# Performance work log

Measured on AMD Instinct MI355X. Metric: run time of the kernel, lower is better.

The kernel has to match this reference:

```python
import jax, jax.numpy as jnp
import numpy as np

N_NODES = 50000
N_EDGES = 500000
IN_CH = 2
HID = 64
OUT_CH = 64
H1 = 4
H2 = 1
EDGE_DIM = 2


def _glorot(key, shape):
    fan_in, fan_out = shape[0], shape[1]
    lim = jnp.sqrt(6.0 / (fan_in + fan_out))
    return jax.random.uniform(key, shape, jnp.float32, -lim, lim)


def setup_inputs() -> dict:
    key = jax.random.key(0)
    ks = jax.random.split(key, 16)
    x = jax.random.uniform(ks[0], (N_NODES, IN_CH), jnp.float32)
    edge_index = jax.random.randint(ks[1], (2, N_EDGES), 0, N_NODES, dtype=jnp.int64)
    edge_attr = jax.random.uniform(ks[2], (N_EDGES, EDGE_DIM), jnp.float32)
    batch = jnp.zeros((N_NODES,), jnp.int32)
    # conv1 params (GATv2: lin_l, lin_r with bias, lin_edge no bias, att, out bias)
    W1l = _glorot(ks[3], (IN_CH, H1 * HID)); b1l = jnp.zeros((H1 * HID,), jnp.float32)
    W1r = _glorot(ks[4], (IN_CH, H1 * HID)); b1r = jnp.zeros((H1 * HID,), jnp.float32)
    W1e = _glorot(ks[5], (EDGE_DIM, H1 * HID))
    att1 = _glorot(ks[6], (H1, HID))
    bias1 = jnp.zeros((H1 * HID,), jnp.float32)
    # conv2 params
    W2l = _glorot(ks[7], (H1 * HID, H2 * OUT_CH)); b2l = jnp.zeros((H2 * OUT_CH,), jnp.float32)
    W2r = _glorot(ks[8], (H1 * HID, H2 * OUT_CH)); b2r = jnp.zeros((H2 * OUT_CH,), jnp.float32)
    W2e = _glorot(ks[9], (EDGE_DIM, H2 * OUT_CH))
    att2 = _glorot(ks[10], (H2, OUT_CH))
    bias2 = jnp.zeros((H2 * OUT_CH,), jnp.float32)
    return dict(x=x, edge_attr=edge_attr,
                W1l=W1l, b1l=b1l, W1r=W1r, b1r=b1r, W1e=W1e, att1=att1, bias1=bias1,
                W2l=W2l, b2l=b2l, W2r=W2r, b2r=b2r, W2e=W2e, att2=att2, bias2=bias2,
                edge_index=edge_index, batch=batch)


def _segment_softmax(alpha, seg, num_segments):
    # alpha: [E, H], seg: [E] destination ids
    amax = jax.ops.segment_max(alpha, seg, num_segments=num_segments)
    amax = jnp.where(jnp.isfinite(amax), amax, 0.0)
    ex = jnp.exp(alpha - amax[seg])
    denom = jax.ops.segment_sum(ex, seg, num_segments=num_segments)
    return ex / (denom[seg] + 1e-16)


def _gatv2_conv(x, edge_index, edge_attr, Wl, bl, Wr, br, We, att, bias, heads, out_c):
    N = x.shape[0]
    src, dst = edge_index[0], edge_index[1]
    # add self loops with fill_value='mean' for edge_attr (PyG default)
    ones = jnp.ones((src.shape[0],), x.dtype)
    deg = jax.ops.segment_sum(ones, dst, num_segments=N)
    loop_attr = jax.ops.segment_sum(edge_attr, dst, num_segments=N) / jnp.maximum(deg, 1.0)[:, None]
    loops = jnp.arange(N, dtype=src.dtype)
    src = jnp.concatenate([src, loops])
    dst = jnp.concatenate([dst, loops])
    ea = jnp.concatenate([edge_attr, loop_attr], axis=0)
    xl = (x @ Wl + bl).reshape(N, heads, out_c)   # source-side transform
    xr = (x @ Wr + br).reshape(N, heads, out_c)   # target-side transform
    ee = (ea @ We).reshape(-1, heads, out_c)
    e = jax.nn.leaky_relu(xl[src] + xr[dst] + ee, 0.2)   # [E', H, C]
    alpha = jnp.einsum('ehc,hc->eh', e, att)
    alpha = _segment_softmax(alpha, dst, N)
    out = jax.ops.segment_sum(xl[src] * alpha[..., None], dst, num_segments=N)
    return out.reshape(N, heads * out_c) + bias


def reference(x, edge_attr, W1l, b1l, W1r, b1r, W1e, att1, bias1,
              W2l, b2l, W2r, b2r, W2e, att2, bias2, edge_index, batch):
    h = jax.nn.elu(_gatv2_conv(x, edge_index, edge_attr, W1l, b1l, W1r, b1r, W1e, att1, bias1, H1, HID))
    # dropout skipped (eval mode)
    h = _gatv2_conv(h, edge_index, edge_attr, W2l, b2l, W2r, b2r, W2e, att2, bias2, H2, OUT_CH)
    # global_mean_pool over batch (single graph -> [1, OUT_CH])
    nb = 1
    cnt = jax.ops.segment_sum(jnp.ones((h.shape[0],), h.dtype), batch, num_segments=nb)
    pooled = jax.ops.segment_sum(h, batch, num_segments=nb) / jnp.maximum(cnt, 1.0)[:, None]
    return pooled
```

## Files before the change

kernel.cpp:

```cpp
#include <hip/hip_runtime.h>
#include <hip/hip_bf16.h>

#define N_NODES 50000
#define N_EDGES 500000
#define E_AUG   (N_EDGES + N_NODES)
#define NH1 4
#define HID 64
#define C2  64

#define NBUCK  196
#define BNODES 256
#define BCAP   4096

#define NL2B    2048
#define L2CHUNK 272
#define L2BINS  320

typedef unsigned int uint32;
typedef unsigned short ushort16;
typedef __attribute__((ext_vector_type(8))) short short8v;
typedef __attribute__((ext_vector_type(4))) float f32x4;

__device__ __forceinline__ ushort16 f2bf(float f) {
    union { float f; uint32 u; } v; v.f = f;
    uint32 u = v.u + (0x7FFFu + ((v.u >> 16) & 1u));
    return (ushort16)(u >> 16);
}
__device__ __forceinline__ float bf2f(ushort16 h) {
    union { uint32 u; float f; } v; v.u = ((uint32)h) << 16;
    return v.f;
}


__global__ void zero_bcnt_kernel(int* __restrict__ bcnt) {
    if (threadIdx.x < 256) bcnt[threadIdx.x] = 0;
}


#define PACK_BLOCKS 128
#define HIST_BLOCKS ((N_EDGES / 4 + 255) / 256)

__global__ void pass1_kernel(const int* __restrict__ ei, const float* __restrict__ ea,
                             const float* __restrict__ W1l, const float* __restrict__ b1l,
                             const float* __restrict__ W1r, const float* __restrict__ b1r,
                             const float* __restrict__ W1e, const float* __restrict__ att1,
                             const float* __restrict__ bias1,
                             const float* __restrict__ W2l, const float* __restrict__ W2r,
                             float* __restrict__ Wpack, float* __restrict__ Apack,
                             float4* __restrict__ wpk4, ushort16* __restrict__ Wt,
                             int4* __restrict__ stage, int* __restrict__ bcnt) {
    const int tid = threadIdx.x;
    if (blockIdx.x < PACK_BLOCKS) {
        int t = blockIdx.x * 256 + tid;
        if (blockIdx.x == 0) {
            if (tid < 256) {
                int h = tid >> 6, hc = tid;
                float* wp = &Wpack[((tid & 63) * 4 + h) * 8];
                wp[0] = W1l[hc];       wp[1] = W1l[256 + hc];
                wp[2] = W1r[hc];       wp[3] = W1r[256 + hc];
                wp[4] = W1e[hc];       wp[5] = W1e[256 + hc];
                wp[6] = b1l[hc] + b1r[hc];
                wp[7] = 0.4f * att1[hc];
                wpk4[hc] = make_float4(W1l[hc], W1l[256 + hc], b1l[hc] + bias1[hc], 0.0f);
            }
            if (tid < 28) {
                int h = tid / 7, comp = tid % 7;
                float s = 0.0f;
                for (int c = 0; c < 64; ++c) {
                    int hc = h * 64 + c;
                    float m;
                    switch (comp) {
                        case 0: m = W1l[hc]; break;
                        case 1: m = W1l[256 + hc]; break;
                        case 2: m = W1r[hc]; break;
                        case 3: m = W1r[256 + hc]; break;
                        case 4: m = W1e[hc]; break;
                        case 5: m = W1e[256 + hc]; break;
                        default: m = b1l[hc] + b1r[hc]; break;
                    }
                    s += att1[hc] * m;
                }
                Apack[h * 8 + comp] = 0.6f * s;
            }
        }
        if (t < 128 * 256) {
            int c = t & 127, k = t >> 7;
            float w = (c < 64) ? W2l[k * 64 + c] : W2r[k * 64 + (c - 64)];
            Wt[c * 256 + k] = f2bf(w);
        }
    } else {
        __shared__ int lbc[NBUCK];
        __shared__ int lbase[NBUCK];
        if (tid < NBUCK) lbc[tid] = 0;
        __syncthreads();

        const int e0 = ((blockIdx.x - PACK_BLOCKS) * 256 + tid) * 4;
        int4 rec[4]; int bket[4], lofs[4];
        bool val[4];
        #pragma unroll
        for (int j = 0; j < 4; ++j) {
            const int e = e0 + j;
            val[j] = (e < N_EDGES);
            if (val[j]) {
                int s = ei[e], d = ei[N_EDGES + e];
                float2 a = *(const float2*)&ea[2 * e];
                rec[j].x = s; rec[j].y = d;
                rec[j].z = __float_as_int(a.x); rec[j].w = __float_as_int(a.y);
                bket[j] = d >> 8;
                lofs[j] = atomicAdd(&lbc[bket[j]], 1);
            }
        }
        __syncthreads();
        if (tid < NBUCK) lbase[tid] = lbc[tid] ? atomicAdd(&bcnt[tid], lbc[tid]) : 0;
        __syncthreads();
        #pragma unroll
        for (int j = 0; j < 4; ++j)
            if (val[j])
                stage[bket[j] * BCAP + lbase[bket[j]] + lofs[j]] = rec[j];
    }
}


__global__ void bscan_kernel(const int* __restrict__ bcnt, int* __restrict__ bbase,
                             int* __restrict__ offs) {
    __shared__ int s[256];
    int tid = threadIdx.x;
    int nodec = (tid < NBUCK) ? min(BNODES, N_NODES - tid * BNODES) : 0;
    int v = (tid < NBUCK) ? bcnt[tid] + nodec : 0;
    s[tid] = v;
    __syncthreads();
    for (int off = 1; off < 256; off <<= 1) {
        int t = (tid >= off) ? s[tid - off] : 0;
        __syncthreads();
        s[tid] += t;
        __syncthreads();
    }
    if (tid < NBUCK) bbase[tid] = s[tid] - v;
    if (tid == 0) offs[N_NODES] = E_AUG;
}


__global__ __launch_bounds__(256) void buildk_kernel(
    const int4* __restrict__ stage, const int* __restrict__ bcnt,
    const int* __restrict__ bbase,
    int* __restrict__ offs, float* __restrict__ den,
    int4* __restrict__ epk, int* __restrict__ e_src) {
    __shared__ int bins[256];
    __shared__ float ls0[256], ls1[256];
    __shared__ int scan[256];
    __shared__ int cursor[256];
    const int tid = threadIdx.x, bk = blockIdx.x;
    bins[tid] = 0; ls0[tid] = 0.0f; ls1[tid] = 0.0f;
    __syncthreads();

    const int n_ = bcnt[bk];
    const int4* sb = stage + (size_t)bk * BCAP;
    for (int i = tid; i < n_; i += 256) {
        int4 r = sb[i];
        int li = r.y & 255;
        atomicAdd(&bins[li], 1);
        atomicAdd(&ls0[li], __int_as_float(r.z));
        atomicAdd(&ls1[li], __int_as_float(r.w));
    }
    __syncthreads();

    const int node = bk * BNODES + tid;
    const int v = (node < N_NODES) ? bins[tid] + 1 : 0;
    scan[tid] = v;
    __syncthreads();
    for (int off = 1; off < 256; off <<= 1) {
        int t = (tid >= off) ? scan[tid - off] : 0;
        __syncthreads();
        scan[tid] += t;
        __syncthreads();
    }
    const int o = bbase[bk] + scan[tid] - v;
    if (node < N_NODES) {
        offs[node] = o;
        den[node] = 0.0f;
        float dgf = (float)max(bins[tid], 1);
        int4 sl;
        sl.x = node; sl.y = node;
        sl.z = __float_as_int(ls0[tid] / dgf);
        sl.w = __float_as_int(ls1[tid] / dgf);
        epk[o] = sl;
        e_src[o] = node;
    }
    cursor[tid] = o + 1;
    __syncthreads();

    for (int i = tid; i < n_; i += 256) {
        int4 r = sb[i];
        int pos = atomicAdd(&cursor[r.y & 255], 1);
        epk[pos] = r;
        e_src[pos] = r.x;
    }
}


__global__ __launch_bounds__(256) void l1_alpha_kernel(
    const float* __restrict__ x, const int4* __restrict__ epk,
    const float* __restrict__ Wpack, const float* __restrict__ Apack,
    float* __restrict__ alpha1) {
    __shared__ float sWp[2048];
    __shared__ float sA[32];
    const int tid = threadIdx.x;
    for (int i = tid; i < 2048; i += 256) sWp[i] = Wpack[i];
    if (tid < 32) sA[tid] = Apack[tid];
    __syncthreads();

    const int e0 = (blockIdx.x * 256 + tid) * 2;
    if (e0 >= E_AUG) return;

    const int4 v0 = epk[e0];
    const int4 v1 = epk[e0 + 1];

    float u0[2], u1[2], u2[2], u3[2], u4[2], u5[2];
    {
        const float2 xs0 = *(const float2*)&x[2 * v0.x];
        const float2 xd0 = *(const float2*)&x[2 * v0.y];
        const float2 xs1 = *(const float2*)&x[2 * v1.x];
        const float2 xd1 = *(const float2*)&x[2 * v1.y];
        u0[0] = xs0.x; u1[0] = xs0.y; u2[0] = xd0.x; u3[0] = xd0.y;
        u4[0] = __int_as_float(v0.z); u5[0] = __int_as_float(v0.w);
        u0[1] = xs1.x; u1[1] = xs1.y; u2[1] = xd1.x; u3[1] = xd1.y;
        u4[1] = __int_as_float(v1.z); u5[1] = __int_as_float(v1.w);
    }

    float p[4][2];
    #pragma unroll
    for (int h = 0; h < 4; ++h) {
        const float a0 = sA[h * 8], a1 = sA[h * 8 + 1], a2 = sA[h * 8 + 2],
                    a3 = sA[h * 8 + 3], a4 = sA[h * 8 + 4], a5 = sA[h * 8 + 5],
                    a6 = sA[h * 8 + 6];
        #pragma unroll
        for (int j = 0; j < 2; ++j)
            p[h][j] = fmaf(u0[j], a0, fmaf(u1[j], a1, fmaf(u2[j], a2,
                      fmaf(u3[j], a3, fmaf(u4[j], a4, fmaf(u5[j], a5, a6))))));
    }

    for (int c = 0; c < 64; ++c) {
        const float* wp = &sWp[c * 32];
        #pragma unroll
        for (int h = 0; h < 4; ++h) {
            const float4 wa = *(const float4*)&wp[h * 8];
            const float4 wb = *(const float4*)&wp[h * 8 + 4];
            #pragma unroll
            for (int j = 0; j < 2; ++j) {
                float t = fmaf(u0[j], wa.x,
                          fmaf(u1[j], wa.y,
                          fmaf(u2[j], wa.z,
                          fmaf(u3[j], wa.w,
                          fmaf(u4[j], wb.x,
                          fmaf(u5[j], wb.y, wb.z))))));
                p[h][j] = fmaf(fabsf(t), wb.w, p[h][j]);
            }
        }
    }

    #pragma unroll
    for (int h = 0; h < 4; ++h)
        *(float2*)&alpha1[(size_t)h * E_AUG + e0] =
            make_float2(__expf(p[h][0]), __expf(p[h][1]));
}


__global__ __launch_bounds__(256) void l1out_fused_kernel(
    const float* __restrict__ x, const int* __restrict__ offs,
    const int* __restrict__ e_src, const float* __restrict__ alpha1,
    const float4* __restrict__ wpk4, const ushort16* __restrict__ Wt,
    const float* __restrict__ b2l, const float* __restrict__ b2r,
    ushort16* __restrict__ xl2b, ushort16* __restrict__ xr2b) {
    __shared__ short hlds[64 * 256];
    __shared__ float4 swpk[256];
    const int tid = threadIdx.x;
    const int n0 = blockIdx.x * 64;
    const int lane = tid & 63, w = tid >> 6;

    swpk[tid] = wpk4[tid];

    const int nl = tid >> 2, head = tid & 3;
    const int node = n0 + nl;
    float S1 = 0.0f, S2 = 0.0f;
    if (node < N_NODES) {
        const int beg = offs[node], end = offs[node + 1];
        const float* ap = alpha1 + (size_t)head * E_AUG;
        float den = 0.0f, s1 = 0.0f, s2 = 0.0f;
        for (int e = beg; e < end; ++e) {
            float wt = ap[e];
            int s = e_src[e];
            float2 xs = *(const float2*)&x[2 * s];
            den += wt;
            s1 = fmaf(wt, xs.x, s1);
            s2 = fmaf(wt, xs.y, s2);
        }
        float inv = 1.0f / (den + 1e-16f);
        S1 = s1 * inv;
        S2 = s2 * inv;
    }
    __syncthreads();

    {
        const int kseg = head * 64;
        const int swz = (nl & 7) << 3;
        for (int i = 0; i < 8; ++i) {
            short8v hv;
            #pragma unroll
            for (int j = 0; j < 8; ++j) {
                float4 wv = swpk[kseg + i * 8 + j];
                float g = fmaf(wv.x, S1, fmaf(wv.y, S2, wv.z));
                g = g > 0.0f ? g : (__expf(g) - 1.0f);
                hv[j] = (short)f2bf(g);
            }
            *(short8v*)&hlds[(nl * 256 + kseg + i * 8) ^ swz] = hv;
        }
    }

    short8v bfrag[2][8];
    {
        const int bc = w * 32 + (lane & 15);
        const int k0 = (lane >> 4) * 8;
        #pragma unroll
        for (int ct = 0; ct < 2; ++ct)
            #pragma unroll
            for (int kb = 0; kb < 8; ++kb)
                bfrag[ct][kb] = *(const short8v*)&Wt[(size_t)(bc + ct * 16) * 256 + kb * 32 + k0];
    }
    __syncthreads();

    f32x4 acc[4][2];
    #pragma unroll
    for (int rt = 0; rt < 4; ++rt)
        #pragma unroll
        for (int ct = 0; ct < 2; ++ct)
            acc[rt][ct] = (f32x4){0.0f, 0.0f, 0.0f, 0.0f};

    const int arow = lane & 15, ak0 = (lane >> 4) * 8;
    #pragma unroll
    for (int rt = 0; rt < 4; ++rt) {
        const int n = rt * 16 + arow;
        const int swz = (n & 7) << 3;
        #pragma unroll
        for (int kb = 0; kb < 8; ++kb) {
            short8v a = *(const short8v*)&hlds[(n * 256 + kb * 32 + ak0) ^ swz];
            acc[rt][0] = __builtin_amdgcn_mfma_f32_16x16x32_bf16(a, bfrag[0][kb], acc[rt][0], 0, 0, 0);
            acc[rt][1] = __builtin_amdgcn_mfma_f32_16x16x32_bf16(a, bfrag[1][kb], acc[rt][1], 0, 0, 0);
        }
    }

    #pragma unroll
    for (int ct = 0; ct < 2; ++ct) {
        const int c = w * 32 + ct * 16 + (lane & 15);
        const bool isL = (c < 64);
        const int cc = isL ? c : c - 64;
        const float bias = isL ? b2l[cc] : b2r[cc];
        ushort16* dst = isL ? xl2b : xr2b;
        #pragma unroll
        for (int rt = 0; rt < 4; ++rt)
            #pragma unroll
            for (int r = 0; r < 4; ++r) {
                int nn = n0 + rt * 16 + (lane >> 4) * 4 + r;
                if (nn < N_NODES) dst[nn * 64 + cc] = f2bf(acc[rt][ct][r] + bias);
            }
    }
}


__global__ __launch_bounds__(256) void l2_logit_kernel(
    const ushort16* __restrict__ xl2b, const ushort16* __restrict__ xr2b,
    const int4* __restrict__ epk,
    const float* __restrict__ W2e, const float* __restrict__ att2,
    float* __restrict__ alpha2, float* __restrict__ den) {
    __shared__ float sWe[128], satt[64];
    __shared__ float bins[L2BINS];
    const int tid = threadIdx.x;
    if (tid < 128) sWe[tid] = W2e[tid];
    if (tid < 64) satt[tid] = att2[tid];
    for (int i = tid; i < L2BINS; i += 256) bins[i] = 0.0f;
    const int base = blockIdx.x * L2CHUNK;
    const int d_first = epk[min(base, E_AUG - 1)].y;
    __syncthreads();

    const int lane = tid & 63, w = tid >> 6;
    const int cl = lane & 15, g = lane >> 4;
    const uint32* xlp = (const uint32*)xl2b;
    const uint32* xrp = (const uint32*)xr2b;

    for (int it = 0; it < L2CHUNK / 16; ++it) {
        const int e = base + it * 16 + w * 4 + g;
        if (e < E_AUG) {
            const int4 v = epk[e];
            const float ae0 = __int_as_float(v.z), ae1 = __int_as_float(v.w);
            float acc = 0.0f;
            #pragma unroll
            for (int q = 0; q < 2; ++q) {
                const int c2 = cl + q * 16;
                const uint32 ul = xlp[v.x * 32 + c2];
                const uint32 ur = xrp[v.y * 32 + c2];
                const int c0 = 2 * c2, c1 = 2 * c2 + 1;
                float xl0 = bf2f((ushort16)(ul & 0xffff)), xl1 = bf2f((ushort16)(ul >> 16));
                float xr0 = bf2f((ushort16)(ur & 0xffff)), xr1 = bf2f((ushort16)(ur >> 16));
                float t0 = xl0 + xr0 + fmaf(ae0, sWe[c0], ae1 * sWe[64 + c0]);
                float t1 = xl1 + xr1 + fmaf(ae0, sWe[c1], ae1 * sWe[64 + c1]);
                t0 = t0 > 0.0f ? t0 : 0.2f * t0;
                t1 = t1 > 0.0f ? t1 : 0.2f * t1;
                acc = fmaf(t0, satt[c0], fmaf(t1, satt[c1], acc));
            }
            #pragma unroll
            for (int off = 8; off; off >>= 1) acc += __shfl_xor(acc, off);
            if (cl == 0) {
                float wv = __expf(acc);
                alpha2[e] = wv;
                int rel = v.y - d_first;
                if (rel < L2BINS) atomicAdd(&bins[rel], wv);
                else atomicAdd(&den[v.y], wv);
            }
        }
    }
    __syncthreads();
    for (int i = tid; i < L2BINS; i += 256) {
        float b = bins[i];
        int node = d_first + i;
        if (b != 0.0f && node < N_NODES) atomicAdd(&den[node], b);
    }
}


__global__ __launch_bounds__(256) void l2_pool_kernel(
    const ushort16* __restrict__ xl2b, const int4* __restrict__ epk,
    const float* __restrict__ alpha2, const float* __restrict__ den,
    float* __restrict__ pblock) {
    __shared__ float sp[16][64];
    const int tid = threadIdx.x;
    const int lane = tid & 63, w = tid >> 6;
    const int cl = lane & 15, g = lane >> 4;
    const int slot = w * 4 + g;
    const int base = blockIdx.x * L2CHUNK;
    const uint32* xlp = (const uint32*)xl2b;

    float a0 = 0.0f, a1 = 0.0f, a2 = 0.0f, a3 = 0.0f;
    for (int it = 0; it < L2CHUNK / 16; ++it) {
        const int e = base + it * 16 + w * 4 + g;
        if (e < E_AUG) {
            const int4 v = epk[e];
            const float coef = alpha2[e] / (den[v.y] + 1e-16f);
            const uint32 u0 = xlp[v.x * 32 + cl];
            const uint32 u1 = xlp[v.x * 32 + cl + 16];
            a0 = fmaf(coef, bf2f((ushort16)(u0 & 0xffff)), a0);
            a1 = fmaf(coef, bf2f((ushort16)(u0 >> 16)), a1);
            a2 = fmaf(coef, bf2f((ushort16)(u1 & 0xffff)), a2);
            a3 = fmaf(coef, bf2f((ushort16)(u1 >> 16)), a3);
        }
    }
    sp[slot][2 * cl] = a0;
    sp[slot][2 * cl + 1] = a1;
    sp[slot][2 * cl + 32] = a2;
    sp[slot][2 * cl + 33] = a3;
    __syncthreads();
    if (tid < 64) {
        float s = 0.0f;
        #pragma unroll
        for (int i = 0; i < 16; ++i) s += sp[i][tid];
        pblock[blockIdx.x * 64 + tid] = s;
    }
}


__global__ __launch_bounds__(256) void pool_partial_kernel(const float* __restrict__ pblock,
                                                           float* __restrict__ pfin) {
    __shared__ float s[256];
    int tid = threadIdx.x;
    int l = tid & 63, q = tid >> 6;
    float local = 0.0f;
    for (int r = blockIdx.x * 4 + q; r < NL2B; r += 64 * 4)
        local += pblock[r * 64 + l];
    s[tid] = local;
    __syncthreads();
    if (tid < 64) {
        float v = s[tid] + s[tid + 64] + s[tid + 128] + s[tid + 192];
        pfin[blockIdx.x * 64 + tid] = v;
    }
}

__global__ __launch_bounds__(256) void pool_final2_kernel(const float* __restrict__ pfin,
                                                          const float* __restrict__ bias2,
                                                          float* __restrict__ d_out) {
    __shared__ float s[256];
    int tid = threadIdx.x;
    int l = tid & 63, q = tid >> 6;
    float local = 0.0f;
    for (int r = q; r < 64; r += 4)
        local += pfin[r * 64 + l];
    s[tid] = local;
    __syncthreads();
    if (tid < 64) {
        float v = s[tid] + s[tid + 64] + s[tid + 128] + s[tid + 192];
        d_out[tid] = v * (1.0f / N_NODES) + bias2[tid];
    }
}


extern "C" void kernel_launch(void* const* d_in, const int* in_sizes, int n_in,
                              void* d_out, int out_size, void* d_ws, size_t ws_size,
                              hipStream_t stream) {
    const float* x     = (const float*)d_in[0];
    const float* eattr = (const float*)d_in[1];
    const float* W1l   = (const float*)d_in[2];
    const float* b1l   = (const float*)d_in[3];
    const float* W1r   = (const float*)d_in[4];
    const float* b1r   = (const float*)d_in[5];
    const float* W1e   = (const float*)d_in[6];
    const float* att1  = (const float*)d_in[7];
    const float* bias1 = (const float*)d_in[8];
    const float* W2l   = (const float*)d_in[9];
    const float* b2l   = (const float*)d_in[10];
    const float* W2r   = (const float*)d_in[11];
    const float* b2r   = (const float*)d_in[12];
    const float* W2e   = (const float*)d_in[13];
    const float* att2  = (const float*)d_in[14];
    const float* bias2 = (const float*)d_in[15];
    const int*   ei    = (const int*)d_in[16];
    float* out = (float*)d_out;

    char* p = (char*)d_ws;
    auto alloc = [&](size_t bytes) -> void* {
        void* r = (void*)p;
        p += (bytes + 255) & ~(size_t)255;
        return r;
    };
    int*   bcnt   = (int*)alloc(256 * 4);
    int*   bbase  = (int*)alloc(256 * 4);
    int*   offs   = (int*)alloc((N_NODES + 1) * 4);
    float* den    = (float*)alloc(N_NODES * 4);
    int4*  stage  = (int4*)alloc((size_t)NBUCK * BCAP * 16);
    int4*  epk    = (int4*)alloc((size_t)E_AUG * 16);
    int*   e_src  = (int*)alloc(E_AUG * 4);
    float* alpha1 = (float*)alloc((size_t)E_AUG * 4 * 4);
    float* alpha2 = (float*)alloc((size_t)E_AUG * 4);
    float* Wpack  = (float*)alloc(256 * 8 * 4);
    float* Apack  = (float*)alloc(32 * 4);
    float4* wpk4  = (float4*)alloc(256 * 16);
    ushort16* Wt  = (ushort16*)alloc(128 * 256 * 2);
    ushort16* xl2b = (ushort16*)alloc((size_t)N_NODES * C2 * 2);
    ushort16* xr2b = (ushort16*)alloc((size_t)N_NODES * C2 * 2);
    float* pblock = (float*)alloc((size_t)NL2B * 64 * 4);
    float* pfin   = (float*)alloc((size_t)64 * 64 * 4);

    zero_bcnt_kernel<<<1, 256, 0, stream>>>(bcnt);

    pass1_kernel<<<PACK_BLOCKS + HIST_BLOCKS, 256, 0, stream>>>(
        ei, eattr, W1l, b1l, W1r, b1r, W1e, att1, bias1, W2l, W2r,
        Wpack, Apack, wpk4, Wt, stage, bcnt);

    bscan_kernel<<<1, 256, 0, stream>>>(bcnt, bbase, offs);

    buildk_kernel<<<NBUCK, 256, 0, stream>>>(stage, bcnt, bbase, offs, den, epk, e_src);

    l1_alpha_kernel<<<(E_AUG / 2 + 255) / 256, 256, 0, stream>>>(x, epk, Wpack, Apack,
                                                                 alpha1);

    l1out_fused_kernel<<<(N_NODES + 63) / 64, 256, 0, stream>>>(x, offs, e_src, alpha1,
                                                                wpk4, Wt, b2l, b2r,
                                                                xl2b, xr2b);

    l2_logit_kernel<<<NL2B, 256, 0, stream>>>(xl2b, xr2b, epk, W2e, att2, alpha2, den);

    l2_pool_kernel<<<NL2B, 256, 0, stream>>>(xl2b, epk, alpha2, den, pblock);

    pool_partial_kernel<<<64, 256, 0, stream>>>(pblock, pfin);
    pool_final2_kernel<<<1, 256, 0, stream>>>(pfin, bias2, out);
}
```

Before: 179.8 us.

## Fuse layer-1 attention logits into edge bucketing pass and self-loops into aggregation

Computes the layer-1 per-edge exp-logits for all four heads inside the bucketing pass and carries them through the CSR build as a packed float4 array. Self-loop logits are now computed directly in the node aggregation kernel, so the separate l1_alpha kernel goes away. Weight packing and the zeroing of the bucket counter are split into their own prep kernel, which runs ahead of the bucketing pass. This saves a kernel launch and a re-read of epk with scattered x gathers. The cost is an extra 16-byte staging write and read per edge, plus more shared memory and a longer per-thread workload in the pass1 and l1out kernels.

New measurement: 206.6 us. 1.15x slower.

```diff
diff --git a/kernel.cpp b/kernel.cpp
--- a/kernel.cpp
+++ b/kernel.cpp
@@ -32,92 +32,123 @@
 }
 
 
-__global__ void zero_bcnt_kernel(int* __restrict__ bcnt) {
-    if (threadIdx.x < 256) bcnt[threadIdx.x] = 0;
-}
-
-
-#define PACK_BLOCKS 128
+__global__ void prep_kernel(const float* __restrict__ W1l, const float* __restrict__ b1l,
+                            const float* __restrict__ W1r, const float* __restrict__ b1r,
+                            const float* __restrict__ W1e, const float* __restrict__ att1,
+                            const float* __restrict__ bias1,
+                            const float* __restrict__ W2l, const float* __restrict__ W2r,
+                            float* __restrict__ Wpack, float* __restrict__ Apack,
+                            float4* __restrict__ wpk4, ushort16* __restrict__ Wt,
+                            int* __restrict__ bcnt) {
+    const int tid = threadIdx.x;
+    int t = blockIdx.x * 256 + tid;
+    if (blockIdx.x == 0) {
+        bcnt[tid] = 0;
+        {
+            int h = tid >> 6, hc = tid;
+            float* wp = &Wpack[((tid & 63) * 4 + h) * 8];
+            wp[0] = W1l[hc];       wp[1] = W1l[256 + hc];
+            wp[2] = W1r[hc];       wp[3] = W1r[256 + hc];
+            wp[4] = W1e[hc];       wp[5] = W1e[256 + hc];
+            wp[6] = b1l[hc] + b1r[hc];
+            wp[7] = 0.4f * att1[hc];
+            wpk4[hc] = make_float4(W1l[hc], W1l[256 + hc], b1l[hc] + bias1[hc], 0.0f);
+        }
+        if (tid < 28) {
+            int h = tid / 7, comp = tid % 7;
+            float s = 0.0f;
+            for (int c = 0; c < 64; ++c) {
+                int hc = h * 64 + c;
+                float m;
+                switch (comp) {
+                    case 0: m = W1l[hc]; break;
+                    case 1: m = W1l[256 + hc]; break;
+                    case 2: m = W1r[hc]; break;
+                    case 3: m = W1r[256 + hc]; break;
+                    case 4: m = W1e[hc]; break;
+                    case 5: m = W1e[256 + hc]; break;
+                    default: m = b1l[hc] + b1r[hc]; break;
+                }
+                s += att1[hc] * m;
+            }
+            Apack[h * 8 + comp] = 0.6f * s;
+        }
+    }
+    if (t < 128 * 256) {
+        int c = t & 127, k = t >> 7;
+        float w = (c < 64) ? W2l[k * 64 + c] : W2r[k * 64 + (c - 64)];
+        Wt[c * 256 + k] = f2bf(w);
+    }
+}
+
+
 #define HIST_BLOCKS ((N_EDGES / 4 + 255) / 256)
 
-__global__ void pass1_kernel(const int* __restrict__ ei, const float* __restrict__ ea,
-                             const float* __restrict__ W1l, const float* __restrict__ b1l,
-                             const float* __restrict__ W1r, const float* __restrict__ b1r,
-                             const float* __restrict__ W1e, const float* __restrict__ att1,
-                             const float* __restrict__ bias1,
-                             const float* __restrict__ W2l, const float* __restrict__ W2r,
-                             float* __restrict__ Wpack, float* __restrict__ Apack,
-                             float4* __restrict__ wpk4, ushort16* __restrict__ Wt,
-                             int4* __restrict__ stage, int* __restrict__ bcnt) {
+__global__ __launch_bounds__(256) void pass1_kernel(
+    const int* __restrict__ ei, const float* __restrict__ ea,
+    const float* __restrict__ x,
+    const float* __restrict__ Wpack, const float* __restrict__ Apack,
+    int4* __restrict__ st_meta, float4* __restrict__ st_alpha,
+    int* __restrict__ bcnt) {
+    __shared__ float sWp[2048];
+    __shared__ float sA[32];
+    __shared__ int lbc[NBUCK];
+    __shared__ int lbase[NBUCK];
     const int tid = threadIdx.x;
-    if (blockIdx.x < PACK_BLOCKS) {
-        int t = blockIdx.x * 256 + tid;
-        if (blockIdx.x == 0) {
-            if (tid < 256) {
-                int h = tid >> 6, hc = tid;
-                float* wp = &Wpack[((tid & 63) * 4 + h) * 8];
-                wp[0] = W1l[hc];       wp[1] = W1l[256 + hc];
-                wp[2] = W1r[hc];       wp[3] = W1r[256 + hc];
-                wp[4] = W1e[hc];       wp[5] = W1e[256 + hc];
-                wp[6] = b1l[hc] + b1r[hc];
-                wp[7] = 0.4f * att1[hc];
-                wpk4[hc] = make_float4(W1l[hc], W1l[256 + hc], b1l[hc] + bias1[hc], 0.0f);
+    for (int i = tid; i < 2048; i += 256) sWp[i] = Wpack[i];
+    if (tid < 32) sA[tid] = Apack[tid];
+    if (tid < NBUCK) lbc[tid] = 0;
+    __syncthreads();
+
+    const int e0 = (blockIdx.x * 256 + tid) * 4;
+    int4 rec[4]; float4 al[4]; int bket[4], lofs[4];
+    bool val[4];
+    #pragma unroll
+    for (int j = 0; j < 4; ++j) {
+        const int e = e0 + j;
+        val[j] = (e < N_EDGES);
+        if (val[j]) {
+            const int s = ei[e], d = ei[N_EDGES + e];
+            const float2 a = *(const float2*)&ea[2 * e];
+            rec[j].x = s; rec[j].y = d;
+            rec[j].z = __float_as_int(a.x); rec[j].w = __float_as_int(a.y);
+            bket[j] = d >> 8;
+            lofs[j] = atomicAdd(&lbc[bket[j]], 1);
+
+            const float2 xs = *(const float2*)&x[2 * s];
+            const float2 xd = *(const float2*)&x[2 * d];
+            const float u0 = xs.x, u1 = xs.y, u2 = xd.x, u3 = xd.y, u4 = a.x, u5 = a.y;
+
+            float p[4];
+            #pragma unroll
+            for (int h = 0; h < 4; ++h)
+                p[h] = fmaf(u0, sA[h * 8], fmaf(u1, sA[h * 8 + 1], fmaf(u2, sA[h * 8 + 2],
+                       fmaf(u3, sA[h * 8 + 3], fmaf(u4, sA[h * 8 + 4],
+                       fmaf(u5, sA[h * 8 + 5], sA[h * 8 + 6]))))));
+            for (int c = 0; c < 64; ++c) {
+                const float* wp = &sWp[c * 32];
+                #pragma unroll
+                for (int h = 0; h < 4; ++h) {
+                    const float4 wa = *(const float4*)&wp[h * 8];
+                    const float4 wb = *(const float4*)&wp[h * 8 + 4];
+                    float tt = fmaf(u0, wa.x, fmaf(u1, wa.y, fmaf(u2, wa.z,
+                               fmaf(u3, wa.w, fmaf(u4, wb.x, fmaf(u5, wb.y, wb.z))))));
+                    p[h] = fmaf(fabsf(tt), wb.w, p[h]);
+                }
             }
-            if (tid < 28) {
-                int h = tid / 7, comp = tid % 7;
-                float s = 0.0f;
-                for (int c = 0; c < 64; ++c) {
-                    int hc = h * 64 + c;
-                    float m;
-                    switch (comp) {
-                        case 0: m = W1l[hc]; break;
-                        case 1: m = W1l[256 + hc]; break;
-                        case 2: m = W1r[hc]; break;
-                        case 3: m = W1r[256 + hc]; break;
-                        case 4: m = W1e[hc]; break;
-                        case 5: m = W1e[256 + hc]; break;
-                        default: m = b1l[hc] + b1r[hc]; break;
-                    }
-                    s += att1[hc] * m;
-                }
-                Apack[h * 8 + comp] = 0.6f * s;
-            }
-        }
-        if (t < 128 * 256) {
-            int c = t & 127, k = t >> 7;
-            float w = (c < 64) ? W2l[k * 64 + c] : W2r[k * 64 + (c - 64)];
-            Wt[c * 256 + k] = f2bf(w);
-        }
-    } else {
-        __shared__ int lbc[NBUCK];
-        __shared__ int lbase[NBUCK];
-        if (tid < NBUCK) lbc[tid] = 0;
-        __syncthreads();
-
-        const int e0 = ((blockIdx.x - PACK_BLOCKS) * 256 + tid) * 4;
-        int4 rec[4]; int bket[4], lofs[4];
-        bool val[4];
-        #pragma unroll
-        for (int j = 0; j < 4; ++j) {
-            const int e = e0 + j;
-            val[j] = (e < N_EDGES);
-            if (val[j]) {
-                int s = ei[e], d = ei[N_EDGES + e];
-                float2 a = *(const float2*)&ea[2 * e];
-                rec[j].x = s; rec[j].y = d;
-                rec[j].z = __float_as_int(a.x); rec[j].w = __float_as_int(a.y);
-                bket[j] = d >> 8;
-                lofs[j] = atomicAdd(&lbc[bket[j]], 1);
-            }
-        }
-        __syncthreads();
-        if (tid < NBUCK) lbase[tid] = lbc[tid] ? atomicAdd(&bcnt[tid], lbc[tid]) : 0;
-        __syncthreads();
-        #pragma unroll
-        for (int j = 0; j < 4; ++j)
-            if (val[j])
-                stage[bket[j] * BCAP + lbase[bket[j]] + lofs[j]] = rec[j];
-    }
+            al[j] = make_float4(__expf(p[0]), __expf(p[1]), __expf(p[2]), __expf(p[3]));
+        }
+    }
+    __syncthreads();
+    if (tid < NBUCK) lbase[tid] = lbc[tid] ? atomicAdd(&bcnt[tid], lbc[tid]) : 0;
+    __syncthreads();
+    #pragma unroll
+    for (int j = 0; j < 4; ++j)
+        if (val[j]) {
+            int pos = bket[j] * BCAP + lbase[bket[j]] + lofs[j];
+            st_meta[pos] = rec[j];
+            st_alpha[pos] = al[j];
+        }
 }
 
 
@@ -141,10 +172,10 @@
 
 
 __global__ __launch_bounds__(256) void buildk_kernel(
-    const int4* __restrict__ stage, const int* __restrict__ bcnt,
-    const int* __restrict__ bbase,
+    const int4* __restrict__ st_meta, const float4* __restrict__ st_alpha,
+    const int* __restrict__ bcnt, const int* __restrict__ bbase,
     int* __restrict__ offs, float* __restrict__ den,
-    int4* __restrict__ epk, int* __restrict__ e_src) {
+    int4* __restrict__ epk, int* __restrict__ e_src, float4* __restrict__ af) {
     __shared__ int bins[256];
     __shared__ float ls0[256], ls1[256];
     __shared__ int scan[256];
@@ -154,7 +185,8 @@
     __syncthreads();
 
     const int n_ = bcnt[bk];
-    const int4* sb = stage + (size_t)bk * BCAP;
+    const int4* sb = st_meta + (size_t)bk * BCAP;
+    const float4* sa = st_alpha + (size_t)bk * BCAP;
     for (int i = tid; i < n_; i += 256) {
         int4 r = sb[i];
         int li = r.y & 255;
@@ -194,100 +226,56 @@
         int pos = atomicAdd(&cursor[r.y & 255], 1);
         epk[pos] = r;
         e_src[pos] = r.x;
-    }
-}
-
-
-__global__ __launch_bounds__(256) void l1_alpha_kernel(
-    const float* __restrict__ x, const int4* __restrict__ epk,
-    const float* __restrict__ Wpack, const float* __restrict__ Apack,
-    float* __restrict__ alpha1) {
-    __shared__ float sWp[2048];
-    __shared__ float sA[32];
-    const int tid = threadIdx.x;
-    for (int i = tid; i < 2048; i += 256) sWp[i] = Wpack[i];
-    if (tid < 32) sA[tid] = Apack[tid];
-    __syncthreads();
-
-    const int e0 = (blockIdx.x * 256 + tid) * 2;
-    if (e0 >= E_AUG) return;
-
-    const int4 v0 = epk[e0];
-    const int4 v1 = epk[e0 + 1];
-
-    float u0[2], u1[2], u2[2], u3[2], u4[2], u5[2];
-    {
-        const float2 xs0 = *(const float2*)&x[2 * v0.x];
-        const float2 xd0 = *(const float2*)&x[2 * v0.y];
-        const float2 xs1 = *(const float2*)&x[2 * v1.x];
-        const float2 xd1 = *(const float2*)&x[2 * v1.y];
-        u0[0] = xs0.x; u1[0] = xs0.y; u2[0] = xd0.x; u3[0] = xd0.y;
-        u4[0] = __int_as_float(v0.z); u5[0] = __int_as_float(v0.w);
-        u0[1] = xs1.x; u1[1] = xs1.y; u2[1] = xd1.x; u3[1] = xd1.y;
-        u4[1] = __int_as_float(v1.z); u5[1] = __int_as_float(v1.w);
-    }
-
-    float p[4][2];
-    #pragma unroll
-    for (int h = 0; h < 4; ++h) {
-        const float a0 = sA[h * 8], a1 = sA[h * 8 + 1], a2 = sA[h * 8 + 2],
-                    a3 = sA[h * 8 + 3], a4 = sA[h * 8 + 4], a5 = sA[h * 8 + 5],
-                    a6 = sA[h * 8 + 6];
-        #pragma unroll
-        for (int j = 0; j < 2; ++j)
-            p[h][j] = fmaf(u0[j], a0, fmaf(u1[j], a1, fmaf(u2[j], a2,
-                      fmaf(u3[j], a3, fmaf(u4[j], a4, fmaf(u5[j], a5, a6))))));
-    }
-
-    for (int c = 0; c < 64; ++c) {
-        const float* wp = &sWp[c * 32];
-        #pragma unroll
-        for (int h = 0; h < 4; ++h) {
-            const float4 wa = *(const float4*)&wp[h * 8];
-            const float4 wb = *(const float4*)&wp[h * 8 + 4];
-            #pragma unroll
-            for (int j = 0; j < 2; ++j) {
-                float t = fmaf(u0[j], wa.x,
-                          fmaf(u1[j], wa.y,
-                          fmaf(u2[j], wa.z,
-                          fmaf(u3[j], wa.w,
-                          fmaf(u4[j], wb.x,
-                          fmaf(u5[j], wb.y, wb.z))))));
-                p[h][j] = fmaf(fabsf(t), wb.w, p[h][j]);
-            }
-        }
-    }
-
-    #pragma unroll
-    for (int h = 0; h < 4; ++h)
-        *(float2*)&alpha1[(size_t)h * E_AUG + e0] =
-            make_float2(__expf(p[h][0]), __expf(p[h][1]));
+        af[pos] = sa[i];
+    }
 }
 
 
 __global__ __launch_bounds__(256) void l1out_fused_kernel(
     const float* __restrict__ x, const int* __restrict__ offs,
-    const int* __restrict__ e_src, const float* __restrict__ alpha1,
+    const int* __restrict__ e_src, const float4* __restrict__ af,
+    const int4* __restrict__ epk,
+    const float* __restrict__ Wpack, const float* __restrict__ Apack,
     const float4* __restrict__ wpk4, const ushort16* __restrict__ Wt,
     const float* __restrict__ b2l, const float* __restrict__ b2r,
     ushort16* __restrict__ xl2b, ushort16* __restrict__ xr2b) {
     __shared__ short hlds[64 * 256];
     __shared__ float4 swpk[256];
+    __shared__ float sWp[2048];
+    __shared__ float sA[32];
     const int tid = threadIdx.x;
     const int n0 = blockIdx.x * 64;
     const int lane = tid & 63, w = tid >> 6;
 
     swpk[tid] = wpk4[tid];
+    for (int i = tid; i < 2048; i += 256) sWp[i] = Wpack[i];
+    if (tid < 32) sA[tid] = Apack[tid];
+    __syncthreads();
 
     const int nl = tid >> 2, head = tid & 3;
     const int node = n0 + nl;
     float S1 = 0.0f, S2 = 0.0f;
     if (node < N_NODES) {
         const int beg = offs[node], end = offs[node + 1];
-        const float* ap = alpha1 + (size_t)head * E_AUG;
-        float den = 0.0f, s1 = 0.0f, s2 = 0.0f;
-        for (int e = beg; e < end; ++e) {
-            float wt = ap[e];
+        const float2 xn = *(const float2*)&x[2 * node];
+        const int4 se = epk[beg];
+        const float u0 = xn.x, u1 = xn.y, u4 = __int_as_float(se.z), u5 = __int_as_float(se.w);
+        float ps = fmaf(u0, sA[head * 8] + sA[head * 8 + 2],
+                   fmaf(u1, sA[head * 8 + 1] + sA[head * 8 + 3],
+                   fmaf(u4, sA[head * 8 + 4], fmaf(u5, sA[head * 8 + 5], sA[head * 8 + 6]))));
+        for (int c = 0; c < 64; ++c) {
+            const float* wp = &sWp[c * 32 + head * 8];
+            const float4 wa = *(const float4*)wp;
+            const float4 wb = *(const float4*)(wp + 4);
+            float tt = fmaf(u0, wa.x + wa.z, fmaf(u1, wa.y + wa.w,
+                       fmaf(u4, wb.x, fmaf(u5, wb.y, wb.z))));
+            ps = fmaf(fabsf(tt), wb.w, ps);
+        }
+        float selfw = __expf(ps);
+        float den = selfw, s1 = selfw * u0, s2 = selfw * u1;
+        const float* afp = (const float*)af;
+        for (int e = beg + 1; e < end; ++e) {
+            float wt = afp[4 * e + head];
             int s = e_src[e];
             float2 xs = *(const float2*)&x[2 * s];
             den += wt;
@@ -298,7 +286,6 @@
         S1 = s1 * inv;
         S2 = s2 * inv;
     }
-    __syncthreads();
 
     {
         const int kseg = head * 64;
@@ -532,10 +519,11 @@
     int*   bbase  = (int*)alloc(256 * 4);
     int*   offs   = (int*)alloc((N_NODES + 1) * 4);
     float* den    = (float*)alloc(N_NODES * 4);
-    int4*  stage  = (int4*)alloc((size_t)NBUCK * BCAP * 16);
+    int4*  st_meta  = (int4*)alloc((size_t)NBUCK * BCAP * 16);
+    float4* st_alpha = (float4*)alloc((size_t)NBUCK * BCAP * 16);
     int4*  epk    = (int4*)alloc((size_t)E_AUG * 16);
     int*   e_src  = (int*)alloc(E_AUG * 4);
-    float* alpha1 = (float*)alloc((size_t)E_AUG * 4 * 4);
+    float4* af    = (float4*)alloc((size_t)E_AUG * 16);
     float* alpha2 = (float*)alloc((size_t)E_AUG * 4);
     float* Wpack  = (float*)alloc(256 * 8 * 4);
     float* Apack  = (float*)alloc(32 * 4);
@@ -546,22 +534,19 @@
     float* pblock = (float*)alloc((size_t)NL2B * 64 * 4);
     float* pfin   = (float*)alloc((size_t)64 * 64 * 4);
 
-    zero_bcnt_kernel<<<1, 256, 0, stream>>>(bcnt);
-
-    pass1_kernel<<<PACK_BLOCKS + HIST_BLOCKS, 256, 0, stream>>>(
-        ei, eattr, W1l, b1l, W1r, b1r, W1e, att1, bias1, W2l, W2r,
-        Wpack, Apack, wpk4, Wt, stage, bcnt);
+    prep_kernel<<<128, 256, 0, stream>>>(W1l, b1l, W1r, b1r, W1e, att1, bias1, W2l, W2r,
+                                         Wpack, Apack, wpk4, Wt, bcnt);
+
+    pass1_kernel<<<HIST_BLOCKS, 256, 0, stream>>>(ei, eattr, x, Wpack, Apack,
+                                                  st_meta, st_alpha, bcnt);
 
     bscan_kernel<<<1, 256, 0, stream>>>(bcnt, bbase, offs);
 
-    buildk_kernel<<<NBUCK, 256, 0, stream>>>(stage, bcnt, bbase, offs, den, epk, e_src);
-
-    l1_alpha_kernel<<<(E_AUG / 2 + 255) / 256, 256, 0, stream>>>(x, epk, Wpack, Apack,
-                                                                 alpha1);
-
-    l1out_fused_kernel<<<(N_NODES + 63) / 64, 256, 0, stream>>>(x, offs, e_src, alpha1,
-                                                                wpk4, Wt, b2l, b2r,
-                                                                xl2b, xr2b);
+    buildk_kernel<<<NBUCK, 256, 0, stream>>>(st_meta, st_alpha, bcnt, bbase,
+                                             offs, den, epk, e_src, af);
+
+    l1out_fused_kernel<<<(N_NODES + 63) / 64, 256, 0, stream>>>(
+        x, offs, e_src, af, epk, Wpack, Apack, wpk4, Wt, b2l, b2r, xl2b, xr2b);
 
     l2_logit_kernel<<<NL2B, 256, 0, stream>>>(xl2b, xr2b, epk, W2e, att2, alpha2, den);
 
```
